# Kernel tuning notes

Hardware: AMD Instinct MI355X
Metric: run time of the kernel (lower is better)

## Reference

```python
import jax, jax.numpy as jnp
import numpy as np

N = 512          # n_nodes
F = 64           # hidden scalar/vector channels (hidden_irreps 64x0e+64x1o)
S = 5            # num_species
T = 32           # time embedding dim
M = 64           # MLP_irreps 64x0e
L = 2            # num_interactions
AVG = 511.0      # avg_num_neighbors (fully connected)
E = N * (N - 1)


def _sph(v):
    """Real spherical harmonics l=0,1,2 (component norm) of normalized vectors. v: [E,3]."""
    r = jnp.linalg.norm(v, axis=-1, keepdims=True)  # [E,1]
    u = v / r
    x, y, z = u[..., 0], u[..., 1], u[..., 2]
    s3, s5, s15 = 3.0 ** 0.5, 5.0 ** 0.5, 15.0 ** 0.5
    Y0 = jnp.ones_like(x)[..., None]
    Y1 = s3 * u
    Y2 = jnp.stack([s15 * x * y, s15 * y * z, 0.5 * s5 * (3 * z * z - 1.0),
                    s15 * x * z, 0.5 * s15 * (x * x - y * y)], axis=-1)
    return jnp.concatenate([Y0, Y1, Y2], axis=-1), r  # [E,9], [E,1]


def setup_inputs() -> dict:
    key = jax.random.key(0)
    ks = jax.random.split(key, 16)
    snd, rcv = np.nonzero(~np.eye(N, dtype=bool))  # fully-connected, no self loops
    return dict(
        positions=jax.random.normal(ks[0], (N, 3), jnp.float32),
        node_features=jax.random.randint(ks[1], (N,), 1, S + 1, jnp.int32),
        time_embedding=jax.random.normal(ks[2], (T,), jnp.float32),
        senders=jnp.asarray(snd, jnp.int32),
        receivers=jnp.asarray(rcv, jnp.int32),
        W_embed=jax.random.normal(ks[3], (S + T, F)) * 0.1,
        b_embed=jnp.zeros((F,)),
        W_lin=jax.random.normal(ks[4], (L, 3, F, F)) / jnp.sqrt(float(F)),
        W_e1=jax.random.normal(ks[5], (L, 1, 32)),
        b_e1=jnp.zeros((L, 32)),
        W_e2=jax.random.normal(ks[6], (L, 32, F * 6)) * 0.05,
        Wp0=jax.random.normal(ks[7], (L, S, F, 6)) * 0.1,
        Wp1=jax.random.normal(ks[8], (L, S, F, 3)) * 0.1,
        Wr1=jax.random.normal(ks[9], (L, F, M)) / jnp.sqrt(float(F)),
        br1=jnp.zeros((L, M)),
        Wr2s=jax.random.normal(ks[10], (L, M, 16)) * 0.1,
        Wr2g=jax.random.normal(ks[11], (L, M, F)) * 0.1,
    )


def reference(positions, node_features, time_embedding, senders, receivers,
              W_embed, b_embed, W_lin, W_e1, b_e1, W_e2, Wp0, Wp1, Wr1, br1, Wr2s, Wr2g):
    species = node_features - 1                                  # ints in [0,S)
    onehot = jax.nn.one_hot(species, S, dtype=positions.dtype)   # /normalization_factor=1
    te = jnp.tile(time_embedding, (N, 1))
    h = jnp.concatenate([onehot, te], axis=-1) @ W_embed + b_embed  # embedding Dense -> [N,F]
    node_feats = jnp.zeros((N, F, 9), positions.dtype).at[:, :, 0].set(h)
    pos0 = positions
    pos = positions
    for l in range(L):
        vec = pos[receivers] - pos[senders]                      # [E,3]
        Y, lengths = _sph(vec)                                   # SH of edge dirs, edge lengths
        # per-l channel-mixing linear on node feats
        x0 = jnp.einsum('nf,fg->ng', node_feats[:, :, 0], W_lin[l, 0])
        x1 = jnp.einsum('nfm,fg->ngm', node_feats[:, :, 1:4], W_lin[l, 1])
        x2 = jnp.einsum('nfm,fg->ngm', node_feats[:, :, 4:9], W_lin[l, 2])
        s0, s1, s2 = x0[senders], x1[senders], x2[senders]       # gather sender feats
        # edge-length MLP producing per-channel per-CG-path weights
        he = jax.nn.silu(lengths @ W_e1[l] + b_e1[l])            # [E,32]
        w = (he @ W_e2[l]).reshape(-1, F, 6)                     # 6 TP paths
        Y1 = Y[:, None, 1:4]
        Y2c = Y[:, None, 4:9]
        # CG tensor-product paths: 0x0->0, 0x1->1, 0x2->2, 1x1->0, 1x1->1, 2x2->0
        m0 = (w[..., 0] * s0 * Y[:, 0:1]
              + w[..., 3] * jnp.sum(s1 * Y1, -1)
              + w[..., 5] * jnp.sum(s2 * Y2c, -1))               # [E,F]
        m1 = w[..., 1, None] * s0[..., None] * Y1 + w[..., 4, None] * jnp.cross(s1, Y1)
        m2 = w[..., 2, None] * s0[..., None] * Y2c
        msg = jnp.concatenate([m0[..., None], m1, m2], axis=-1)  # [E,F,9]
        A = jax.ops.segment_sum(msg, receivers, num_segments=N) / AVG  # scatter-aggregate
        # EquivariantProductBasisBlock: species-weighted symmetric contractions (correlation 3)
        A0, A1, A2 = A[:, :, 0], A[:, :, 1:4], A[:, :, 4:9]
        n1 = jnp.sum(A1 * A1, -1)
        n2 = jnp.sum(A2 * A2, -1)
        t0 = jnp.stack([A0, A0 * A0, A0 ** 3, n1, n2, A0 * n1], axis=-1)
        w0 = Wp0[l][species]                                     # [N,F,6]
        w1 = Wp1[l][species]                                     # [N,F,3]
        out0 = jnp.sum(t0 * w0, -1)                              # [N,F] scalars
        gpoly = w1[..., 0] + w1[..., 1] * A0 + w1[..., 2] * A0 * A0
        out1 = gpoly[..., None] * A1                             # [N,F,3] vectors
        node_feats = (jnp.zeros((N, F, 9), positions.dtype)
                      .at[:, :, 0].set(out0).at[:, :, 1:4].set(out1))
        # NonLinearReadoutBlock: gated vector readout (scalar outputs are discarded upstream)
        hr = jax.nn.silu(out0 @ Wr1[l] + br1[l])
        gate = hr @ Wr2g[l]                                      # [N,F]
        vec_out = jnp.einsum('nf,nfc->nc', gate, out1)           # [N,3] many_body_vectors
        pos = pos + vec_out
    return (pos - pos0)[:, :3]                                    # final_scaling = 1.0
```

## Files before the change

### kernel.cpp

```cpp
#include <hip/hip_runtime.h>
#include <hip/hip_bf16.h>

using bf16 = __hip_bfloat16;
using bf16x8 = __attribute__((ext_vector_type(8))) short;
using f32x4  = __attribute__((ext_vector_type(4))) float;

#define NN 512
#define NS 511

enum : int {
  WS_FLAG = 0,
  WS_X0S  = 16,
  WS_POS  = 336,
  WS_POS2 = 1872,
  WS_DELTA= 3408,
  WS_XS1  = 4960,
};

__device__ __forceinline__ short f2b(float x) {
  unsigned u = __builtin_bit_cast(unsigned, x);
  unsigned r = (u + 0x7fffu + ((u >> 16) & 1u)) >> 16;
  return (short)r;
}

__device__ __forceinline__ float ld(const void* p, int i, int isf32) {
  if (isf32) return ((const float*)p)[i];
  return __bfloat162float(((const bf16*)p)[i]);
}

__global__ __launch_bounds__(256) void k_pre(
    const void* __restrict__ positions, const void* __restrict__ te,
    const void* __restrict__ W_embed, const void* __restrict__ b_embed,
    const void* __restrict__ W_lin, float* __restrict__ ws) {
  const int b = blockIdx.x, t = threadIdx.x;
  __shared__ int flag_s;
  __shared__ float tvp[4][64];
  __shared__ float hst[64];
  __shared__ float xp[4][64];
  if (t < 64) {
    int cnt = 0;
    #pragma unroll
    for (int kq = 0; kq < 4; ++kq) {
      float v = __bfloat162float(((const bf16*)W_embed)[t + kq * 64]);
      float av = fabsf(v);
      cnt += (v == v && av > 1e-8f && av < 1e4f) ? 1 : 0;
    }
    #pragma unroll
    for (int off = 32; off > 0; off >>= 1) cnt += __shfl_down(cnt, off);
    if (t == 0) flag_s = (cnt >= 240) ? 0 : 1;
  }
  __syncthreads();
  const int isf32 = flag_s;

  if (b == 5) {
    if (t == 0) ((int*)ws)[WS_FLAG] = isf32;
    for (int idx = t; idx < NN * 3; idx += 256)
      ws[WS_POS + idx] = ld(positions, idx, isf32);
    return;
  }
  {
    int q = t & 63, kc = t >> 6;
    float ptv = 0.f;
    #pragma unroll
    for (int k = kc * 8; k < kc * 8 + 8; ++k)
      ptv += ld(te, k, isf32) * ld(W_embed, (5 + k) * 64 + q, isf32);
    tvp[kc][q] = ptv;
  }
  __syncthreads();
  if (t < 64)
    hst[t] = tvp[0][t] + tvp[1][t] + tvp[2][t] + tvp[3][t] +
             ld(b_embed, t, isf32) + ld(W_embed, b * 64 + t, isf32);
  __syncthreads();
  {
    int f = t & 63, qc = t >> 6;
    float px = 0.f;
    #pragma unroll
    for (int q2 = qc * 16; q2 < qc * 16 + 16; ++q2)
      px += hst[q2] * ld(W_lin, q2 * 64 + f, isf32);
    xp[qc][f] = px;
  }
  __syncthreads();
  if (t < 64)
    ws[WS_X0S + b * 64 + t] = xp[0][t] + xp[1][t] + xp[2][t] + xp[3][t];
}

template <int L>
__global__ __launch_bounds__(256) void k_edgenode(
    const int* __restrict__ nodef, const void* __restrict__ W_lin,
    const void* __restrict__ W_e1, const void* __restrict__ b_e1,
    const void* __restrict__ W_e2, const void* __restrict__ Wp0,
    const void* __restrict__ Wp1, const void* __restrict__ Wr1,
    const void* __restrict__ br1, const void* __restrict__ Wr2g,
    float* __restrict__ ws, void* __restrict__ out) {
  constexpr int HAS1 = L;
  constexpr int K = HAS1 ? 5 : 3;
  constexpr int N = K * 64;
  const int j = blockIdx.x;
  const int t = threadIdx.x;
  const int lane = t & 63;
  const int wave = t >> 6;
  const int quad = lane >> 4;
  const int lo = lane & 15;

  __shared__ short Bhi[N * 40];
  __shared__ float red[4][64][9];
  __shared__ float Af[64][9];
  __shared__ float s0l[64];
  __shared__ float o1l[3][64];
  __shared__ float hl[64];
  __shared__ float X0l[320];

  const int isf32 = ((const int*)ws)[WS_FLAG];

  {
    for (int idx = t; idx < N * 32; idx += 256) {
      int n = idx >> 5, h = idx & 31;
      int kp = n >> 6, f = n & 63;
      int src = (L * 32 + h) * 384 + f * 6 + kp;
      short bits;
      if (isf32) bits = f2b(((const float*)W_e2)[src]);
      else       bits = ((const short*)W_e2)[src];
      Bhi[n * 40 + h] = bits;
    }
    if (!HAS1) {
      for (int idx = t; idx < 320; idx += 256) X0l[idx] = ws[WS_X0S + idx];
    }
  }
  const float* pos = ws + (L ? WS_POS2 : WS_POS);
  const f32x4* xs = (const f32x4*)(ws + WS_XS1);
  float we1v[8], be1v[8];
  #pragma unroll
  for (int i = 0; i < 8; ++i) {
    we1v[i] = ld(W_e1, L * 32 + quad * 8 + i, isf32);
    be1v[i] = ld(b_e1, L * 32 + quad * 8 + i, isf32);
  }
  const float pjx = pos[j * 3 + 0], pjy = pos[j * 3 + 1], pjz = pos[j * 3 + 2];

  const float s3 = 1.7320508075688772f;
  const float s5h = 1.118033988749895f;
  const float s15 = 3.872983346207417f;
  const float s15h = 1.9364916731037085f;

  float acc[9][4] = {};
  __syncthreads();

  #pragma unroll 1
  for (int stile = wave; stile < 32; stile += 4) {
    bf16x8 af;
    {
      int ida = stile * 16 + lo;
      int ia = ida + (ida >= j);
      if (ia > 511) ia = 511;
      float pix = pos[ia * 3 + 0], piy = pos[ia * 3 + 1], piz = pos[ia * 3 + 2];
      float vx = pjx - pix, vy = pjy - piy, vz = pjz - piz;
      float r = sqrtf(vx * vx + vy * vy + vz * vz);
      #pragma unroll
      for (int i = 0; i < 8; ++i) {
        float x = r * we1v[i] + be1v[i];
        float he = x / (1.f + __expf(-x));
        af[i] = f2b(he);
      }
    }
    float Y1r[4][3], Y2r[4][5];
    int ir[4], sp4[4];
    bool vld[4];
    #pragma unroll
    for (int r4 = 0; r4 < 4; ++r4) {
      int idx = stile * 16 + quad * 4 + r4;
      vld[r4] = idx < NS;
      int i = idx + (idx >= j);
      if (i > 511) i = 511;
      ir[r4] = i;
      if (!HAS1) sp4[r4] = nodef[i] - 1;
      float pix = pos[i * 3 + 0], piy = pos[i * 3 + 1], piz = pos[i * 3 + 2];
      float vx = pjx - pix, vy = pjy - piy, vz = pjz - piz;
      float r2 = vx * vx + vy * vy + vz * vz;
      float rinv = r2 > 0.f ? rsqrtf(r2) : 0.f;
      float ux = vx * rinv, uy = vy * rinv, uz = vz * rinv;
      Y1r[r4][0] = s3 * ux; Y1r[r4][1] = s3 * uy; Y1r[r4][2] = s3 * uz;
      Y2r[r4][0] = s15 * ux * uy;
      Y2r[r4][1] = s15 * uy * uz;
      Y2r[r4][2] = s5h * (3.f * uz * uz - 1.f);
      Y2r[r4][3] = s15 * ux * uz;
      Y2r[r4][4] = s15h * (ux * ux - uy * uy);
    }
    #pragma unroll
    for (int ft = 0; ft < 4; ++ft) {
      int fcol = ft * 16 + lo;
      f32x4 xv[4];
      if (HAS1) {
        #pragma unroll
        for (int r4 = 0; r4 < 4; ++r4) xv[r4] = xs[ir[r4] * 64 + fcol];
      } else {
        #pragma unroll
        for (int r4 = 0; r4 < 4; ++r4) {
          f32x4 v = {X0l[sp4[r4] * 64 + fcol], 0.f, 0.f, 0.f};
          xv[r4] = v;
        }
      }
      f32x4 C[K];
      #pragma unroll
      for (int kp = 0; kp < K; ++kp) {
        const bf16x8 bh = *(const bf16x8*)&Bhi[(kp * 64 + fcol) * 40 + quad * 8];
        f32x4 c = {0.f, 0.f, 0.f, 0.f};
        C[kp] = __builtin_amdgcn_mfma_f32_16x16x32_bf16(af, bh, c, 0, 0, 0);
      }
      #pragma unroll
      for (int r4 = 0; r4 < 4; ++r4) {
        if (vld[r4]) {
          float s0 = xv[r4].x;
          float w0 = C[0][r4], w1 = C[1][r4], w2 = C[2][r4];
          if (HAS1) {
            float s1x = xv[r4].y, s1y = xv[r4].z, s1z = xv[r4].w;
            float w3 = C[3][r4], w4 = C[4][r4];
            float d1 = s1x * Y1r[r4][0] + s1y * Y1r[r4][1] + s1z * Y1r[r4][2];
            float cx = s1y * Y1r[r4][2] - s1z * Y1r[r4][1];
            float cy = s1z * Y1r[r4][0] - s1x * Y1r[r4][2];
            float cz = s1x * Y1r[r4][1] - s1y * Y1r[r4][0];
            acc[0][ft] += w0 * s0 + w3 * d1;
            float t1 = w1 * s0;
            acc[1][ft] += t1 * Y1r[r4][0] + w4 * cx;
            acc[2][ft] += t1 * Y1r[r4][1] + w4 * cy;
            acc[3][ft] += t1 * Y1r[r4][2] + w4 * cz;
          } else {
            acc[0][ft] += w0 * s0;
            float t1 = w1 * s0;
            acc[1][ft] += t1 * Y1r[r4][0];
            acc[2][ft] += t1 * Y1r[r4][1];
            acc[3][ft] += t1 * Y1r[r4][2];
          }
          float t2 = w2 * s0;
          acc[4][ft] += t2 * Y2r[r4][0];
          acc[5][ft] += t2 * Y2r[r4][1];
          acc[6][ft] += t2 * Y2r[r4][2];
          acc[7][ft] += t2 * Y2r[r4][3];
          acc[8][ft] += t2 * Y2r[r4][4];
        }
      }
    }
  }

  #pragma unroll
  for (int c = 0; c < 9; ++c)
    #pragma unroll
    for (int ft = 0; ft < 4; ++ft) {
      float v = acc[c][ft];
      v += __shfl_xor(v, 16);
      v += __shfl_xor(v, 32);
      acc[c][ft] = v;
    }
  if (quad == 0) {
    #pragma unroll
    for (int c = 0; c < 9; ++c)
      #pragma unroll
      for (int ft = 0; ft < 4; ++ft)
        red[wave][ft * 16 + lo][c] = acc[c][ft];
  }
  __syncthreads();
  for (int o = t; o < 576; o += 256) {
    int f = o / 9, c = o % 9;
    Af[f][c] = (red[0][f][c] + red[1][f][c] + red[2][f][c] + red[3][f][c]) *
               (1.f / 511.f);
  }
  __syncthreads();

  float out0 = 0.f, o1x = 0.f, o1y = 0.f, o1z = 0.f;
  if (t < 64) {
    int f = t;
    float a[9];
    #pragma unroll
    for (int c = 0; c < 9; ++c) a[c] = Af[f][c];
    int sp = nodef[j] - 1;
    int b0i = ((L * 5 + sp) * 64 + f) * 6;
    int b1i = ((L * 5 + sp) * 64 + f) * 3;
    float A0 = a[0];
    float n1 = a[1] * a[1] + a[2] * a[2] + a[3] * a[3];
    float n2 = a[4] * a[4] + a[5] * a[5] + a[6] * a[6] + a[7] * a[7] + a[8] * a[8];
    float A02 = A0 * A0;
    out0 = ld(Wp0, b0i + 0, isf32) * A0 + ld(Wp0, b0i + 1, isf32) * A02 +
           ld(Wp0, b0i + 2, isf32) * A02 * A0 + ld(Wp0, b0i + 3, isf32) * n1 +
           ld(Wp0, b0i + 4, isf32) * n2 + ld(Wp0, b0i + 5, isf32) * A0 * n1;
    float gp = ld(Wp1, b1i + 0, isf32) + ld(Wp1, b1i + 1, isf32) * A0 +
               ld(Wp1, b1i + 2, isf32) * A02;
    o1x = gp * a[1]; o1y = gp * a[2]; o1z = gp * a[3];
    s0l[f] = out0;
    if (L == 0) { o1l[0][f] = o1x; o1l[1][f] = o1y; o1l[2][f] = o1z; }
  }
  __syncthreads();
  if (t < 64) {
    int f = t;
    if (L == 0) {
      float b0 = 0.f, bx = 0.f, by = 0.f, bz = 0.f;
      #pragma unroll 8
      for (int q = 0; q < 64; ++q) {
        float w0 = ld(W_lin, 3 * 4096 + q * 64 + f, isf32);
        float w1 = ld(W_lin, 4 * 4096 + q * 64 + f, isf32);
        b0 += s0l[q] * w0;
        bx += o1l[0][q] * w1; by += o1l[1][q] * w1; bz += o1l[2][q] * w1;
      }
      f32x4 o = {b0, bx, by, bz};
      *(f32x4*)&ws[WS_XS1 + (j * 64 + f) * 4] = o;
    }
    float hacc = ld(br1, L * 64 + f, isf32);
    #pragma unroll 8
    for (int q = 0; q < 64; ++q)
      hacc += s0l[q] * ld(Wr1, (L * 64 + q) * 64 + f, isf32);
    hl[f] = hacc / (1.f + __expf(-hacc));
  }
  __syncthreads();
  if (t < 64) {
    int f = t;
    float gacc = 0.f;
    #pragma unroll 8
    for (int m = 0; m < 64; ++m)
      gacc += hl[m] * ld(Wr2g, (L * 64 + m) * 64 + f, isf32);
    float px = gacc * o1x, py = gacc * o1y, pz = gacc * o1z;
    #pragma unroll
    for (int off = 32; off > 0; off >>= 1) {
      px += __shfl_down(px, off);
      py += __shfl_down(py, off);
      pz += __shfl_down(pz, off);
    }
    if (f == 0) {
      if (L == 0) {
        ws[WS_DELTA + j * 3 + 0] = px;
        ws[WS_DELTA + j * 3 + 1] = py;
        ws[WS_DELTA + j * 3 + 2] = pz;
        ws[WS_POS2 + j * 3 + 0] = pos[j * 3 + 0] + px;
        ws[WS_POS2 + j * 3 + 1] = pos[j * 3 + 1] + py;
        ws[WS_POS2 + j * 3 + 2] = pos[j * 3 + 2] + pz;
      } else {
        float ox = ws[WS_DELTA + j * 3 + 0] + px;
        float oy = ws[WS_DELTA + j * 3 + 1] + py;
        float oz = ws[WS_DELTA + j * 3 + 2] + pz;
        if (isf32) {
          float* o = (float*)out;
          o[j * 3 + 0] = ox; o[j * 3 + 1] = oy; o[j * 3 + 2] = oz;
        } else {
          bf16* o = (bf16*)out;
          o[j * 3 + 0] = __float2bfloat16(ox);
          o[j * 3 + 1] = __float2bfloat16(oy);
          o[j * 3 + 2] = __float2bfloat16(oz);
        }
      }
    }
  }
}

extern "C" void kernel_launch(void* const* d_in, const int* in_sizes, int n_in,
                              void* d_out, int out_size, void* d_ws, size_t ws_size,
                              hipStream_t stream) {
  const void* positions = d_in[0];
  const int*  nodef     = (const int*)d_in[1];
  const void* te        = d_in[2];
  const void* W_embed   = d_in[5];
  const void* b_embed   = d_in[6];
  const void* W_lin     = d_in[7];
  const void* W_e1      = d_in[8];
  const void* b_e1      = d_in[9];
  const void* W_e2      = d_in[10];
  const void* Wp0       = d_in[11];
  const void* Wp1       = d_in[12];
  const void* Wr1       = d_in[13];
  const void* br1       = d_in[14];
  const void* Wr2g      = d_in[16];
  float* ws = (float*)d_ws;
  (void)in_sizes; (void)n_in; (void)out_size; (void)ws_size;

  k_pre<<<dim3(6), dim3(256), 0, stream>>>(positions, te, W_embed, b_embed,
                                           W_lin, ws);
  k_edgenode<0><<<dim3(512), dim3(256), 0, stream>>>(
      nodef, W_lin, W_e1, b_e1, W_e2, Wp0, Wp1, Wr1, br1, Wr2g, ws, d_out);
  k_edgenode<1><<<dim3(512), dim3(256), 0, stream>>>(
      nodef, W_lin, W_e1, b_e1, W_e2, Wp0, Wp1, Wr1, br1, Wr2g, ws, d_out);
}
```

Before: 187.7 us.

## Split edge/node kernels and halve sender range per block for more parallelism

Splits the fused edge+node kernel into separate edge-aggregation and node-update kernels. The edge kernel now launches two blocks per receiver, each covering half the sender tiles, with waves split by sender and feature halves. Partial sums go to a workspace buffer and the node kernel combines them. This raises block count to fill more CUs and drops the mostly idle single-wave node tail from the edge blocks. In exchange it adds two kernel launches, a global round trip for the partial aggregates, and repeated per-block W_e2 staging into shared memory.

```diff
diff --git a/kernel.cpp b/kernel.cpp
--- a/kernel.cpp
+++ b/kernel.cpp
@@ -15,6 +15,7 @@
   WS_POS2 = 1872,
   WS_DELTA= 3408,
   WS_XS1  = 4960,
+  WS_A    = 136032,
 };
 
 __device__ __forceinline__ short f2b(float x) {
@@ -85,29 +86,25 @@
 }
 
 template <int L>
-__global__ __launch_bounds__(256) void k_edgenode(
-    const int* __restrict__ nodef, const void* __restrict__ W_lin,
-    const void* __restrict__ W_e1, const void* __restrict__ b_e1,
-    const void* __restrict__ W_e2, const void* __restrict__ Wp0,
-    const void* __restrict__ Wp1, const void* __restrict__ Wr1,
-    const void* __restrict__ br1, const void* __restrict__ Wr2g,
-    float* __restrict__ ws, void* __restrict__ out) {
+__global__ __launch_bounds__(256) void k_edge(
+    const int* __restrict__ nodef, const void* __restrict__ W_e1,
+    const void* __restrict__ b_e1, const void* __restrict__ W_e2,
+    float* __restrict__ ws) {
   constexpr int HAS1 = L;
   constexpr int K = HAS1 ? 5 : 3;
   constexpr int N = K * 64;
-  const int j = blockIdx.x;
+  const int j = blockIdx.x & 511;
+  const int half = blockIdx.x >> 9;
   const int t = threadIdx.x;
   const int lane = t & 63;
   const int wave = t >> 6;
+  const int sh = wave >> 1;
+  const int fh = wave & 1;
   const int quad = lane >> 4;
   const int lo = lane & 15;
 
   __shared__ short Bhi[N * 40];
   __shared__ float red[4][64][9];
-  __shared__ float Af[64][9];
-  __shared__ float s0l[64];
-  __shared__ float o1l[3][64];
-  __shared__ float hl[64];
   __shared__ float X0l[320];
 
   const int isf32 = ((const int*)ws)[WS_FLAG];
@@ -141,11 +138,12 @@
   const float s15 = 3.872983346207417f;
   const float s15h = 1.9364916731037085f;
 
-  float acc[9][4] = {};
+  float acc[9][2] = {};
   __syncthreads();
 
   #pragma unroll 1
-  for (int stile = wave; stile < 32; stile += 4) {
+  for (int st = sh; st < 16; st += 2) {
+    const int stile = half * 16 + st;
     bf16x8 af;
     {
       int ida = stile * 16 + lo;
@@ -185,7 +183,8 @@
       Y2r[r4][4] = s15h * (ux * ux - uy * uy);
     }
     #pragma unroll
-    for (int ft = 0; ft < 4; ++ft) {
+    for (int ftl = 0; ftl < 2; ++ftl) {
+      int ft = fh * 2 + ftl;
       int fcol = ft * 16 + lo;
       f32x4 xv[4];
       if (HAS1) {
@@ -217,24 +216,24 @@
             float cx = s1y * Y1r[r4][2] - s1z * Y1r[r4][1];
             float cy = s1z * Y1r[r4][0] - s1x * Y1r[r4][2];
             float cz = s1x * Y1r[r4][1] - s1y * Y1r[r4][0];
-            acc[0][ft] += w0 * s0 + w3 * d1;
+            acc[0][ftl] += w0 * s0 + w3 * d1;
             float t1 = w1 * s0;
-            acc[1][ft] += t1 * Y1r[r4][0] + w4 * cx;
-            acc[2][ft] += t1 * Y1r[r4][1] + w4 * cy;
-            acc[3][ft] += t1 * Y1r[r4][2] + w4 * cz;
+            acc[1][ftl] += t1 * Y1r[r4][0] + w4 * cx;
+            acc[2][ftl] += t1 * Y1r[r4][1] + w4 * cy;
+            acc[3][ftl] += t1 * Y1r[r4][2] + w4 * cz;
           } else {
-            acc[0][ft] += w0 * s0;
+            acc[0][ftl] += w0 * s0;
             float t1 = w1 * s0;
-            acc[1][ft] += t1 * Y1r[r4][0];
-            acc[2][ft] += t1 * Y1r[r4][1];
-            acc[3][ft] += t1 * Y1r[r4][2];
+            acc[1][ftl] += t1 * Y1r[r4][0];
+            acc[2][ftl] += t1 * Y1r[r4][1];
+            acc[3][ftl] += t1 * Y1r[r4][2];
           }
           float t2 = w2 * s0;
-          acc[4][ft] += t2 * Y2r[r4][0];
-          acc[5][ft] += t2 * Y2r[r4][1];
-          acc[6][ft] += t2 * Y2r[r4][2];
-          acc[7][ft] += t2 * Y2r[r4][3];
-          acc[8][ft] += t2 * Y2r[r4][4];
+          acc[4][ftl] += t2 * Y2r[r4][0];
+          acc[5][ftl] += t2 * Y2r[r4][1];
+          acc[6][ftl] += t2 * Y2r[r4][2];
+          acc[7][ftl] += t2 * Y2r[r4][3];
+          acc[8][ftl] += t2 * Y2r[r4][4];
         }
       }
     }
@@ -243,105 +242,114 @@
   #pragma unroll
   for (int c = 0; c < 9; ++c)
     #pragma unroll
-    for (int ft = 0; ft < 4; ++ft) {
-      float v = acc[c][ft];
+    for (int ftl = 0; ftl < 2; ++ftl) {
+      float v = acc[c][ftl];
       v += __shfl_xor(v, 16);
       v += __shfl_xor(v, 32);
-      acc[c][ft] = v;
+      acc[c][ftl] = v;
     }
   if (quad == 0) {
     #pragma unroll
     for (int c = 0; c < 9; ++c)
       #pragma unroll
-      for (int ft = 0; ft < 4; ++ft)
-        red[wave][ft * 16 + lo][c] = acc[c][ft];
+      for (int ftl = 0; ftl < 2; ++ftl)
+        red[wave][(fh * 2 + ftl) * 16 + lo][c] = acc[c][ftl];
   }
   __syncthreads();
   for (int o = t; o < 576; o += 256) {
     int f = o / 9, c = o % 9;
-    Af[f][c] = (red[0][f][c] + red[1][f][c] + red[2][f][c] + red[3][f][c]) *
-               (1.f / 511.f);
-  }
-  __syncthreads();
-
-  float out0 = 0.f, o1x = 0.f, o1y = 0.f, o1z = 0.f;
-  if (t < 64) {
-    int f = t;
-    float a[9];
-    #pragma unroll
-    for (int c = 0; c < 9; ++c) a[c] = Af[f][c];
-    int sp = nodef[j] - 1;
-    int b0i = ((L * 5 + sp) * 64 + f) * 6;
-    int b1i = ((L * 5 + sp) * 64 + f) * 3;
-    float A0 = a[0];
-    float n1 = a[1] * a[1] + a[2] * a[2] + a[3] * a[3];
-    float n2 = a[4] * a[4] + a[5] * a[5] + a[6] * a[6] + a[7] * a[7] + a[8] * a[8];
-    float A02 = A0 * A0;
-    out0 = ld(Wp0, b0i + 0, isf32) * A0 + ld(Wp0, b0i + 1, isf32) * A02 +
-           ld(Wp0, b0i + 2, isf32) * A02 * A0 + ld(Wp0, b0i + 3, isf32) * n1 +
-           ld(Wp0, b0i + 4, isf32) * n2 + ld(Wp0, b0i + 5, isf32) * A0 * n1;
-    float gp = ld(Wp1, b1i + 0, isf32) + ld(Wp1, b1i + 1, isf32) * A0 +
-               ld(Wp1, b1i + 2, isf32) * A02;
-    o1x = gp * a[1]; o1y = gp * a[2]; o1z = gp * a[3];
-    s0l[f] = out0;
-    if (L == 0) { o1l[0][f] = o1x; o1l[1][f] = o1y; o1l[2][f] = o1z; }
-  }
-  __syncthreads();
-  if (t < 64) {
-    int f = t;
+    int b = (f >= 32) ? 1 : 0;
+    ws[WS_A + (half * NN + j) * 576 + f * 9 + c] =
+        red[b][f][c] + red[b + 2][f][c];
+  }
+}
+
+template <int L>
+__global__ __launch_bounds__(64) void k_node(
+    const int* __restrict__ nodef, const void* __restrict__ W_lin,
+    const void* __restrict__ Wp0, const void* __restrict__ Wp1,
+    const void* __restrict__ Wr1, const void* __restrict__ br1,
+    const void* __restrict__ Wr2g, float* __restrict__ ws,
+    void* __restrict__ out) {
+  int n = blockIdx.x, f = threadIdx.x;
+  const int isf32 = ((const int*)ws)[WS_FLAG];
+  const float* Ap0 = ws + WS_A + n * 576 + f * 9;
+  const float* Ap1 = Ap0 + NN * 576;
+  float a[9];
+  #pragma unroll
+  for (int c = 0; c < 9; ++c) a[c] = (Ap0[c] + Ap1[c]) * (1.f / 511.f);
+  int sp = nodef[n] - 1;
+  int b0i = ((L * 5 + sp) * 64 + f) * 6;
+  int b1i = ((L * 5 + sp) * 64 + f) * 3;
+  float A0 = a[0];
+  float n1 = a[1] * a[1] + a[2] * a[2] + a[3] * a[3];
+  float n2 = a[4] * a[4] + a[5] * a[5] + a[6] * a[6] + a[7] * a[7] + a[8] * a[8];
+  float A02 = A0 * A0;
+  float out0 = ld(Wp0, b0i + 0, isf32) * A0 + ld(Wp0, b0i + 1, isf32) * A02 +
+               ld(Wp0, b0i + 2, isf32) * A02 * A0 + ld(Wp0, b0i + 3, isf32) * n1 +
+               ld(Wp0, b0i + 4, isf32) * n2 + ld(Wp0, b0i + 5, isf32) * A0 * n1;
+  float gp = ld(Wp1, b1i + 0, isf32) + ld(Wp1, b1i + 1, isf32) * A0 +
+             ld(Wp1, b1i + 2, isf32) * A02;
+  float o1x = gp * a[1], o1y = gp * a[2], o1z = gp * a[3];
+
+  __shared__ float s0l[64];
+  __shared__ float o1l[3][64];
+  __shared__ float hl[64];
+  s0l[f] = out0;
+  if (L == 0) { o1l[0][f] = o1x; o1l[1][f] = o1y; o1l[2][f] = o1z; }
+  __syncthreads();
+
+  if (L == 0) {
+    float b0 = 0.f, bx = 0.f, by = 0.f, bz = 0.f;
+    #pragma unroll 8
+    for (int q = 0; q < 64; ++q) {
+      float w0 = ld(W_lin, 3 * 4096 + q * 64 + f, isf32);
+      float w1 = ld(W_lin, 4 * 4096 + q * 64 + f, isf32);
+      b0 += s0l[q] * w0;
+      bx += o1l[0][q] * w1; by += o1l[1][q] * w1; bz += o1l[2][q] * w1;
+    }
+    f32x4 o = {b0, bx, by, bz};
+    *(f32x4*)&ws[WS_XS1 + (n * 64 + f) * 4] = o;
+  }
+
+  float hacc = ld(br1, L * 64 + f, isf32);
+  #pragma unroll 8
+  for (int q = 0; q < 64; ++q)
+    hacc += s0l[q] * ld(Wr1, (L * 64 + q) * 64 + f, isf32);
+  float hr = hacc / (1.f + __expf(-hacc));
+  hl[f] = hr;
+  __syncthreads();
+  float gacc = 0.f;
+  #pragma unroll 8
+  for (int m = 0; m < 64; ++m)
+    gacc += hl[m] * ld(Wr2g, (L * 64 + m) * 64 + f, isf32);
+  float px = gacc * o1x, py = gacc * o1y, pz = gacc * o1z;
+  #pragma unroll
+  for (int off = 32; off > 0; off >>= 1) {
+    px += __shfl_down(px, off);
+    py += __shfl_down(py, off);
+    pz += __shfl_down(pz, off);
+  }
+  if (f == 0) {
     if (L == 0) {
-      float b0 = 0.f, bx = 0.f, by = 0.f, bz = 0.f;
-      #pragma unroll 8
-      for (int q = 0; q < 64; ++q) {
-        float w0 = ld(W_lin, 3 * 4096 + q * 64 + f, isf32);
-        float w1 = ld(W_lin, 4 * 4096 + q * 64 + f, isf32);
-        b0 += s0l[q] * w0;
-        bx += o1l[0][q] * w1; by += o1l[1][q] * w1; bz += o1l[2][q] * w1;
-      }
-      f32x4 o = {b0, bx, by, bz};
-      *(f32x4*)&ws[WS_XS1 + (j * 64 + f) * 4] = o;
-    }
-    float hacc = ld(br1, L * 64 + f, isf32);
-    #pragma unroll 8
-    for (int q = 0; q < 64; ++q)
-      hacc += s0l[q] * ld(Wr1, (L * 64 + q) * 64 + f, isf32);
-    hl[f] = hacc / (1.f + __expf(-hacc));
-  }
-  __syncthreads();
-  if (t < 64) {
-    int f = t;
-    float gacc = 0.f;
-    #pragma unroll 8
-    for (int m = 0; m < 64; ++m)
-      gacc += hl[m] * ld(Wr2g, (L * 64 + m) * 64 + f, isf32);
-    float px = gacc * o1x, py = gacc * o1y, pz = gacc * o1z;
-    #pragma unroll
-    for (int off = 32; off > 0; off >>= 1) {
-      px += __shfl_down(px, off);
-      py += __shfl_down(py, off);
-      pz += __shfl_down(pz, off);
-    }
-    if (f == 0) {
-      if (L == 0) {
-        ws[WS_DELTA + j * 3 + 0] = px;
-        ws[WS_DELTA + j * 3 + 1] = py;
-        ws[WS_DELTA + j * 3 + 2] = pz;
-        ws[WS_POS2 + j * 3 + 0] = pos[j * 3 + 0] + px;
-        ws[WS_POS2 + j * 3 + 1] = pos[j * 3 + 1] + py;
-        ws[WS_POS2 + j * 3 + 2] = pos[j * 3 + 2] + pz;
+      ws[WS_DELTA + n * 3 + 0] = px;
+      ws[WS_DELTA + n * 3 + 1] = py;
+      ws[WS_DELTA + n * 3 + 2] = pz;
+      ws[WS_POS2 + n * 3 + 0] = ws[WS_POS + n * 3 + 0] + px;
+      ws[WS_POS2 + n * 3 + 1] = ws[WS_POS + n * 3 + 1] + py;
+      ws[WS_POS2 + n * 3 + 2] = ws[WS_POS + n * 3 + 2] + pz;
+    } else {
+      float ox = ws[WS_DELTA + n * 3 + 0] + px;
+      float oy = ws[WS_DELTA + n * 3 + 1] + py;
+      float oz = ws[WS_DELTA + n * 3 + 2] + pz;
+      if (isf32) {
+        float* o = (float*)out;
+        o[n * 3 + 0] = ox; o[n * 3 + 1] = oy; o[n * 3 + 2] = oz;
       } else {
-        float ox = ws[WS_DELTA + j * 3 + 0] + px;
-        float oy = ws[WS_DELTA + j * 3 + 1] + py;
-        float oz = ws[WS_DELTA + j * 3 + 2] + pz;
-        if (isf32) {
-          float* o = (float*)out;
-          o[j * 3 + 0] = ox; o[j * 3 + 1] = oy; o[j * 3 + 2] = oz;
-        } else {
-          bf16* o = (bf16*)out;
-          o[j * 3 + 0] = __float2bfloat16(ox);
-          o[j * 3 + 1] = __float2bfloat16(oy);
-          o[j * 3 + 2] = __float2bfloat16(oz);
-        }
+        bf16* o = (bf16*)out;
+        o[n * 3 + 0] = __float2bfloat16(ox);
+        o[n * 3 + 1] = __float2bfloat16(oy);
+        o[n * 3 + 2] = __float2bfloat16(oz);
       }
     }
   }
@@ -369,8 +377,10 @@
 
   k_pre<<<dim3(6), dim3(256), 0, stream>>>(positions, te, W_embed, b_embed,
                                            W_lin, ws);
-  k_edgenode<0><<<dim3(512), dim3(256), 0, stream>>>(
-      nodef, W_lin, W_e1, b_e1, W_e2, Wp0, Wp1, Wr1, br1, Wr2g, ws, d_out);
-  k_edgenode<1><<<dim3(512), dim3(256), 0, stream>>>(
-      nodef, W_lin, W_e1, b_e1, W_e2, Wp0, Wp1, Wr1, br1, Wr2g, ws, d_out);
-}
+  k_edge<0><<<dim3(1024), dim3(256), 0, stream>>>(nodef, W_e1, b_e1, W_e2, ws);
+  k_node<0><<<dim3(512), dim3(64), 0, stream>>>(nodef, W_lin, Wp0, Wp1, Wr1,
+                                                br1, Wr2g, ws, d_out);
+  k_edge<1><<<dim3(1024), dim3(256), 0, stream>>>(nodef, W_e1, b_e1, W_e2, ws);
+  k_node<1><<<dim3(512), dim3(64), 0, stream>>>(nodef, W_lin, Wp0, Wp1, Wr1,
+                                                br1, Wr2g, ws, d_out);
+}
```

New measurement: 222.4 us. 1.18x slower.
